# Kernel optimization log

Measured on AMD Instinct MI355X. Metric: run time of the kernel, lower is better.

The kernel has to match this reference:

```python
import jax, jax.numpy as jnp
import numpy as np

D_MODEL = 2048
D_HEAD = 128
N_HEADS = D_MODEL // D_HEAD
SEQ_LENS = (512, 768, 384, 384)  # packed varlen sequences, sum = 2048
L_TOTAL = sum(SEQ_LENS)
EPS = 1e-6


def setup_inputs() -> dict:
    key = jax.random.key(0)
    ks = jax.random.split(key, 8)
    x = jax.random.normal(ks[0], (L_TOTAL, D_MODEL), jnp.float32)
    # Flux-style rope table: pairwise-duplicated cos/sin, pe = concat([cos, sin], -1) -> (L, 2*d_head)
    half = D_HEAD // 2
    pos = np.arange(L_TOTAL, dtype=np.float32)[:, None]
    freqs = 1.0 / (10000.0 ** (np.arange(half, dtype=np.float32) / half))  # (half,)
    ang = pos * freqs[None, :]                      # (L, half)
    cos = np.repeat(np.cos(ang), 2, axis=-1)        # (L, d_head), duplicated per pair
    sin = np.repeat(np.sin(ang), 2, axis=-1)
    pe = jnp.asarray(np.concatenate([cos, sin], axis=-1))  # (L, 2*d_head)
    seq_lens = jnp.asarray(SEQ_LENS, dtype=jnp.int32)
    std = 0.02
    qkv_w = std * jax.random.truncated_normal(ks[1], -2.0, 2.0, (3 * D_MODEL, D_MODEL), jnp.float32)
    qkv_b = jnp.zeros((3 * D_MODEL,), jnp.float32)
    q_scale = jnp.ones((D_HEAD,), jnp.float32)
    k_scale = jnp.ones((D_HEAD,), jnp.float32)
    proj_w = std * jax.random.truncated_normal(ks[2], -2.0, 2.0, (D_MODEL, D_MODEL), jnp.float32)
    proj_b = jnp.zeros((D_MODEL,), jnp.float32)
    return {"x": x, "pe": pe, "seq_lens": seq_lens, "qkv_w": qkv_w, "qkv_b": qkv_b,
            "q_scale": q_scale, "k_scale": k_scale, "proj_w": proj_w, "proj_b": proj_b}


def _rms_norm(t, scale):
    tf = t.astype(jnp.float32)
    rrms = jax.lax.rsqrt(jnp.mean(tf * tf, axis=-1, keepdims=True) + EPS)
    return (tf * rrms * scale).astype(t.dtype)


def _apply_rope(t, pe):
    # t: (L, nh, dh); pe: (L, 2*dh) with pairwise-duplicated cos|sin
    L, nh, dh = t.shape
    c = pe[:, None, 0:dh:2]     # (L, 1, dh/2) per-pair cos
    s = pe[:, None, dh::2]      # (L, 1, dh/2) per-pair sin
    tr = t.reshape(L, nh, dh // 2, 2)
    t1, t2 = tr[..., 0], tr[..., 1]
    out = jnp.stack([t1 * c - t2 * s, t1 * s + t2 * c], axis=-1)
    return out.reshape(L, nh, dh)


def reference(x, pe, seq_lens, qkv_w, qkv_b, q_scale, k_scale, proj_w, proj_b):
    L = x.shape[0]
    qkv = x @ qkv_w.T + qkv_b                      # (L, 3*D)
    q, k, v = jnp.split(qkv, 3, axis=-1)
    q = q.reshape(L, N_HEADS, D_HEAD)
    k = k.reshape(L, N_HEADS, D_HEAD)
    v = v.reshape(L, N_HEADS, D_HEAD)
    q = _rms_norm(q, q_scale)
    k = _rms_norm(k, k_scale)
    q = _apply_rope(q, pe)
    k = _apply_rope(k, pe)
    # block-diagonal (packed varlen) attention
    n = seq_lens.shape[0]
    seg = jnp.repeat(jnp.arange(n, dtype=jnp.int32), seq_lens, total_repeat_length=L)  # (L,)
    mask = seg[:, None] == seg[None, :]            # (L, L) block-diagonal
    scale = 1.0 / jnp.sqrt(jnp.float32(D_HEAD))
    scores = jnp.einsum('lhd,mhd->hlm', q, k) * scale  # (nh, L, L)
    scores = jnp.where(mask[None], scores, jnp.finfo(scores.dtype).min)
    p = jax.nn.softmax(scores, axis=-1)
    out = jnp.einsum('hlm,mhd->lhd', p, v)         # (L, nh, dh)
    out = out.reshape(L, D_MODEL)
    return out @ proj_w.T + proj_b
```

## Files before the change

kernel.cpp:

```cpp
#include <hip/hip_runtime.h>

typedef unsigned short ushort_t;
typedef __attribute__((ext_vector_type(4))) float f4;
typedef __attribute__((ext_vector_type(8))) short s8v;
typedef __attribute__((ext_vector_type(8))) __bf16 bf8v;

#define AS1 __attribute__((address_space(1)))
#define AS3 __attribute__((address_space(3)))

__device__ __forceinline__ void async16(void* lds, const void* g) {
    __builtin_amdgcn_global_load_lds((AS1 const void*)g, (AS3 void*)lds, 16, 0, 0);
}

__device__ __forceinline__ f4 mfma16(s8v a, s8v b, f4 c) {
    return __builtin_amdgcn_mfma_f32_16x16x32_bf16(
        __builtin_bit_cast(bf8v, a), __builtin_bit_cast(bf8v, b), c, 0, 0, 0);
}

__device__ __forceinline__ ushort_t f2bf(float f) {
    unsigned int u = __float_as_uint(f);
    u += 0x7fffu + ((u >> 16) & 1u);
    return (ushort_t)(u >> 16);
}
__device__ __forceinline__ float bf2f(ushort_t u) {
    return __uint_as_float(((unsigned int)u) << 16);
}

#define L_TOT   2048
#define DMODEL  2048
#define DHEAD   128
#define NHEADS  16

__global__ __launch_bounds__(256) void cast_all(const float* __restrict__ x,
                                                const float* __restrict__ w1,
                                                const float* __restrict__ w2,
                                                ushort_t* __restrict__ xo,
                                                ushort_t* __restrict__ w1o,
                                                ushort_t* __restrict__ w2o) {
    int i = blockIdx.x * 256 + threadIdx.x;
    const float* src; ushort_t* dst; int off;
    if (i < 1048576)      { src = x;  dst = xo;  off = 0; }
    else if (i < 4194304) { src = w1; dst = w1o; off = 1048576; }
    else                  { src = w2; dst = w2o; off = 4194304; }
    int j = i - off;
    float4 v = ((const float4*)src)[j];
    ushort4 o;
    o.x = f2bf(v.x); o.y = f2bf(v.y); o.z = f2bf(v.z); o.w = f2bf(v.w);
    ((ushort4*)dst)[j] = o;
}


template <int P>
__device__ __forceinline__ void cluster(f4 (&acc)[8][4], const s8v (&af)[2][2],
                                        const s8v (&bf)[4][2]) {
    __builtin_amdgcn_s_setprio(1);
#pragma unroll
    for (int mm = 0; mm < 2; mm++)
#pragma unroll
        for (int nn = 0; nn < 4; nn++) {
            acc[2 * P + mm][nn] = mfma16(af[mm][0], bf[nn][0], acc[2 * P + mm][nn]);
            acc[2 * P + mm][nn] = mfma16(af[mm][1], bf[nn][1], acc[2 * P + mm][nn]);
        }
    __builtin_amdgcn_s_setprio(0);
}

#define LDF(base, row, oo) (*(const s8v*)&(base)[(row) * 64 + (oo)])

#define STG(dst, gb, Tt, h)                                                              \
    async16(&(dst)[tid * 8 + (2 * (h)) * 4096],                                          \
            (gb) + (size_t)(Tt) * 64 + (size_t)(128 * (h)) * K);                         \
    async16(&(dst)[tid * 8 + (2 * (h) + 1) * 4096],                                      \
            (gb) + (size_t)(Tt) * 64 + (size_t)(128 * (h) + 64) * K);

#define TILE(cur, T)                                                                     \
    {                                                                                    \
        const int Tn1 = ((T) + 1 < NT) ? (T) + 1 : NT - 1;                               \
        const int Tn2 = ((T) + 2 < NT) ? (T) + 2 : NT - 1;                               \
        const ushort_t* fA = stA[cur];                                                   \
        const ushort_t* fB = stB[cur];                                                   \
        s8v bfrag[4][2];                                                                 \
        s8v afrag[2][2];                                                                 \
                                                                  \
        bfrag[0][0] = LDF(fB, brow + 0,  o0); bfrag[0][1] = LDF(fB, brow + 0,  o1);      \
        bfrag[1][0] = LDF(fB, brow + 16, o0); bfrag[1][1] = LDF(fB, brow + 16, o1);      \
        bfrag[2][0] = LDF(fB, brow + 32, o0); bfrag[2][1] = LDF(fB, brow + 32, o1);      \
        bfrag[3][0] = LDF(fB, brow + 48, o0); bfrag[3][1] = LDF(fB, brow + 48, o1);      \
        afrag[0][0] = LDF(fA, arow + 0,  o0); afrag[0][1] = LDF(fA, arow + 0,  o1);      \
        afrag[1][0] = LDF(fA, arow + 16, o0); afrag[1][1] = LDF(fA, arow + 16, o1);      \
        STG(stA[(cur) ^ 1], gA, Tn1, 0)                                                  \
        __builtin_amdgcn_s_barrier();                                                    \
        cluster<0>(acc, afrag, bfrag);                                                   \
        __builtin_amdgcn_s_barrier();                                                    \
                                                                  \
        afrag[0][0] = LDF(fA, arow + 32, o0); afrag[0][1] = LDF(fA, arow + 32, o1);      \
        afrag[1][0] = LDF(fA, arow + 48, o0); afrag[1][1] = LDF(fA, arow + 48, o1);      \
        STG(stA[(cur) ^ 1], gA, Tn1, 1)                                                  \
        __builtin_amdgcn_s_barrier();                                                    \
        cluster<1>(acc, afrag, bfrag);                                                   \
        __builtin_amdgcn_s_barrier();                                                    \
                                                                  \
        afrag[0][0] = LDF(fA, arow + 64, o0); afrag[0][1] = LDF(fA, arow + 64, o1);      \
        afrag[1][0] = LDF(fA, arow + 80, o0); afrag[1][1] = LDF(fA, arow + 80, o1);      \
        STG(stB[cur], gB, Tn2, 0)                                                        \
        __builtin_amdgcn_s_barrier();                                                    \
        cluster<2>(acc, afrag, bfrag);                                                   \
        __builtin_amdgcn_s_barrier();                                                    \
                                                                  \
        afrag[0][0] = LDF(fA, arow + 96,  o0); afrag[0][1] = LDF(fA, arow + 96,  o1);    \
        afrag[1][0] = LDF(fA, arow + 112, o0); afrag[1][1] = LDF(fA, arow + 112, o1);    \
        STG(stB[cur], gB, Tn2, 1)                                                        \
        asm volatile("s_waitcnt vmcnt(4)" ::: "memory");                                 \
        __builtin_amdgcn_sched_barrier(0);                                               \
        __builtin_amdgcn_s_barrier();                                                    \
        cluster<3>(acc, afrag, bfrag);                                                   \
        __builtin_amdgcn_s_barrier();                                                    \
    }

__global__ __launch_bounds__(512, 2) void gemm_qkv256(const ushort_t* __restrict__ A,
                                                      const ushort_t* __restrict__ Bt,
                                                      const float* __restrict__ bias,
                                                      ushort_t* __restrict__ qk_out,
                                                      ushort_t* __restrict__ vt_out,
                                                      int K) {
    __shared__ alignas(16) ushort_t sA[2][16384];
    __shared__ alignas(16) ushort_t sB[2][16384];

    const int tid  = threadIdx.x;
    const int lane = tid & 63;
    const int wave = tid >> 6;
    const int wm = wave >> 2;
    const int wn = wave & 3;
    const int bm = blockIdx.x * 256;
    const int bn = blockIdx.y * 256;
    const bool is_v = blockIdx.y >= 16;
    const int NT = K >> 6;

    const int q15 = lane & 15;
    const int g   = lane >> 4;
    const int l7  = lane & 7;
    const int o0  = ((g    ) ^ l7) * 8;
    const int o1  = ((g + 4) ^ l7) * 8;
    const int arow = wm * 128 + q15;
    const int brow = wn * 64 + q15;

    const int rs  = tid >> 3;
    const int csw = ((tid & 7) ^ (rs & 7)) * 8;
    const ushort_t* Abase = A  + (size_t)(bm + rs) * K + csw;
    const ushort_t* Bbase = Bt + (size_t)(bn + rs) * K + csw;

    ushort_t* stA[2]; ushort_t* stB[2];
    const ushort_t* gA; const ushort_t* gB;
    if (!is_v) { stA[0] = sA[0]; stA[1] = sA[1]; stB[0] = sB[0]; stB[1] = sB[1];
                 gA = Abase; gB = Bbase; }
    else       { stA[0] = sB[0]; stA[1] = sB[1]; stB[0] = sA[0]; stB[1] = sA[1];
                 gA = Bbase; gB = Abase; }

    f4 acc[8][4];
#pragma unroll
    for (int i = 0; i < 8; i++)
#pragma unroll
        for (int j = 0; j < 4; j++) acc[i][j] = (f4){0.f, 0.f, 0.f, 0.f};

    STG(stA[0], gA, 0, 0) STG(stA[0], gA, 0, 1)
    STG(stB[0], gB, 0, 0) STG(stB[0], gB, 0, 1)
    {
        const int T1 = NT > 1 ? 1 : 0;
        STG(stB[1], gB, T1, 0) STG(stB[1], gB, T1, 1)
    }
    asm volatile("s_waitcnt vmcnt(4)" ::: "memory");
    __builtin_amdgcn_sched_barrier(0);
    __builtin_amdgcn_s_barrier();

    for (int T = 0; T < NT; T += 2) {
        TILE(0, T)
        TILE(1, T + 1)
    }

    if (!is_v) {
#pragma unroll
        for (int n = 0; n < 4; n++) {
            int col = bn + wn * 64 + n * 16 + q15;
            float bv = bias[col];
#pragma unroll
            for (int m = 0; m < 8; m++) {
                int r0 = bm + wm * 128 + m * 16 + g * 4;
#pragma unroll
                for (int r = 0; r < 4; r++)
                    qk_out[(size_t)(r0 + r) * 4096 + col] = f2bf(acc[m][n][r] + bv);
            }
        }
    } else {
        const int cb   = (blockIdx.y - 16) * 256 + wm * 128;
        const int tok0 = bm + wn * 64 + q15;
#pragma unroll
        for (int m = 0; m < 8; m++) {
#pragma unroll
            for (int r = 0; r < 4; r++) {
                int c = cb + m * 16 + g * 4 + r;
                float bv = bias[4096 + c];
#pragma unroll
                for (int n = 0; n < 4; n++)
                    vt_out[(size_t)c * L_TOT + tok0 + n * 16] = f2bf(acc[m][n][r] + bv);
            }
        }
    }
}

__global__ __launch_bounds__(256) void gemm_proj(const ushort_t* __restrict__ A,
                                                 const ushort_t* __restrict__ Bt,
                                                 float* __restrict__ Cf,
                                                 int K) {
    __shared__ alignas(16) ushort_t pA[128 * 64];
    __shared__ alignas(16) ushort_t pB[128 * 64];
    const int tid  = threadIdx.x;
    const int lane = tid & 63;
    const int wave = tid >> 6;
    const int wr = (wave >> 1) * 64;
    const int wc = (wave & 1) * 64;
    const int bm = blockIdx.x * 128;
    const int bn = blockIdx.y * 128;

    f4 acc[4][4];
#pragma unroll
    for (int i = 0; i < 4; i++)
#pragma unroll
        for (int j = 0; j < 4; j++) acc[i][j] = (f4){0.f, 0.f, 0.f, 0.f};

    const int rs  = tid >> 3;
    const int csw = ((tid & 7) ^ (rs & 7)) * 8;
    const ushort_t* Abase = A  + (size_t)(bm + rs) * K + csw;
    const ushort_t* Bbase = Bt + (size_t)(bn + rs) * K + csw;
    const int arow = wr + (lane & 15);
    const int brow = wc + (lane & 15);
    const int l7 = lane & 7;
    const int o0 = (((lane >> 4)    ) ^ l7) * 8;
    const int o1 = (((lane >> 4) + 4) ^ l7) * 8;
    const int kbeg = blockIdx.z * (K >> 1);
    const int kend = kbeg + (K >> 1);

    for (int k0 = kbeg; k0 < kend; k0 += 64) {
#pragma unroll
        for (int s = 0; s < 4; s++) {
            async16(&pA[tid * 8 + s * 2048], Abase + k0 + (size_t)(32 * s) * K);
            async16(&pB[tid * 8 + s * 2048], Bbase + k0 + (size_t)(32 * s) * K);
        }
        __syncthreads();

        s8v af[4], bfr[4];
#pragma unroll
        for (int i = 0; i < 4; i++) af[i]  = *(const s8v*)&pA[(arow + i * 16) * 64 + o0];
#pragma unroll
        for (int j = 0; j < 4; j++) bfr[j] = *(const s8v*)&pB[(brow + j * 16) * 64 + o0];
#pragma unroll
        for (int i = 0; i < 4; i++)
#pragma unroll
            for (int j = 0; j < 4; j++) acc[i][j] = mfma16(af[i], bfr[j], acc[i][j]);

#pragma unroll
        for (int i = 0; i < 4; i++) af[i]  = *(const s8v*)&pA[(arow + i * 16) * 64 + o1];
#pragma unroll
        for (int j = 0; j < 4; j++) bfr[j] = *(const s8v*)&pB[(brow + j * 16) * 64 + o1];
#pragma unroll
        for (int i = 0; i < 4; i++)
#pragma unroll
            for (int j = 0; j < 4; j++) acc[i][j] = mfma16(af[i], bfr[j], acc[i][j]);
        __syncthreads();
    }

    const int q = lane & 15;
    const int g = lane >> 4;
    const int crow0 = bm + wr + g * 4;
    const int ccol0 = bn + wc + q;
    float* Cp = Cf + (size_t)blockIdx.z * L_TOT * DMODEL;
#pragma unroll
    for (int j = 0; j < 4; j++) {
        int col = ccol0 + j * 16;
#pragma unroll
        for (int i = 0; i < 4; i++) {
#pragma unroll
            for (int r = 0; r < 4; r++)
                Cp[(size_t)(crow0 + i * 16 + r) * DMODEL + col] = acc[i][j][r];
        }
    }
}

__global__ __launch_bounds__(256) void reduce_bias(const float* __restrict__ part,
                                                   const float* __restrict__ bias,
                                                   float* __restrict__ out) {
    int i = blockIdx.x * 256 + threadIdx.x;
    f4 a = ((const f4*)part)[i];
    f4 b = ((const f4*)(part + (size_t)L_TOT * DMODEL))[i];
    f4 bv = ((const f4*)bias)[i & 511];
    ((f4*)out)[i] = a + b + bv;
}

__global__ __launch_bounds__(256) void norm_rope(const ushort_t* __restrict__ qk,
                                                 const float* __restrict__ pe,
                                                 const float* __restrict__ q_scale,
                                                 const float* __restrict__ k_scale,
                                                 ushort_t* __restrict__ qh,
                                                 ushort_t* __restrict__ kh) {
    int wid  = blockIdx.x * 4 + (threadIdx.x >> 6);
    int lane = threadIdx.x & 63;
    int l = wid >> 4;
    int h = wid & 15;

    const ushort_t* base = qk + (size_t)l * 4096 + h * DHEAD + 2 * lane;
    ushort2 qu = *(const ushort2*)base;
    ushort2 ku = *(const ushort2*)(base + 2048);
    float qvx = bf2f(qu.x), qvy = bf2f(qu.y);
    float kvx = bf2f(ku.x), kvy = bf2f(ku.y);

    float qss = qvx * qvx + qvy * qvy;
    float kss = kvx * kvx + kvy * kvy;
#pragma unroll
    for (int m = 32; m >= 1; m >>= 1) {
        qss += __shfl_xor(qss, m);
        kss += __shfl_xor(kss, m);
    }
    float qr = rsqrtf(qss * (1.0f / DHEAD) + 1e-6f);
    float kr = rsqrtf(kss * (1.0f / DHEAD) + 1e-6f);

    float c = pe[(size_t)l * 256 + 2 * lane];
    float s = pe[(size_t)l * 256 + 128 + 2 * lane];

    float q1 = qvx * qr * q_scale[2 * lane];
    float q2 = qvy * qr * q_scale[2 * lane + 1];
    float k1 = kvx * kr * k_scale[2 * lane];
    float k2 = kvy * kr * k_scale[2 * lane + 1];

    const float sc = 0.08838834764831845f;
    float qo0 = (q1 * c - q2 * s) * sc;
    float qo1 = (q1 * s + q2 * c) * sc;
    float ko0 = k1 * c - k2 * s;
    float ko1 = k1 * s + k2 * c;

    size_t o = ((size_t)h * L_TOT + l) * DHEAD + 2 * lane;
    ushort2 qp, kp;
    qp.x = f2bf(qo0); qp.y = f2bf(qo1);
    kp.x = f2bf(ko0); kp.y = f2bf(ko1);
    *(ushort2*)(qh + o) = qp;
    *(ushort2*)(kh + o) = kp;
}

__global__ __launch_bounds__(256) void attn_kernel(const ushort_t* __restrict__ qh,
                                                   const ushort_t* __restrict__ kh,
                                                   const ushort_t* __restrict__ vt,
                                                   ushort_t* __restrict__ attn_out) {
    __shared__ alignas(16) ushort_t sK[64 * 128];
    __shared__ alignas(16) ushort_t sV[128 * 64];
    __shared__ alignas(16) ushort_t sP[4][16 * 64];

    const int qt = blockIdx.x;
    const int h  = blockIdx.y;
    const int tid = threadIdx.x;
    const int lane = tid & 63;
    const int w = tid >> 6;
    const int qrow0 = qt * 64 + w * 16;

    int q0 = qt * 64;
    int seg_start, seg_end;
    if (q0 < 512)       { seg_start = 0;    seg_end = 512;  }
    else if (q0 < 1280) { seg_start = 512;  seg_end = 1280; }
    else if (q0 < 1664) { seg_start = 1280; seg_end = 1664; }
    else                { seg_start = 1664; seg_end = 2048; }

    const int g = lane >> 4;
    const int q = lane & 15;
    const int qa7 = q & 7;

    const ushort_t* ksrc[4];
    const ushort_t* vsrc[4];
#pragma unroll
    for (int i = 0; i < 4; i++) {
        int p = i * 256 + tid;
        ksrc[i] = kh + ((size_t)h * L_TOT + (p >> 4)) * DHEAD + ((p & 15) ^ ((p >> 4) & 7)) * 8;
        vsrc[i] = vt + ((size_t)h * DHEAD + (p >> 3)) * L_TOT + ((p & 7) ^ ((p >> 3) & 7)) * 8;
    }

    s8v qf[4];
    {
        const ushort_t* qbase = qh + ((size_t)h * L_TOT + qrow0 + q) * DHEAD;
#pragma unroll
        for (int kd = 0; kd < 4; kd++) qf[kd] = *(const s8v*)(qbase + kd * 32 + g * 8);
    }

    f4 o[8];
#pragma unroll
    for (int j = 0; j < 8; j++) o[j] = (f4){0.f, 0.f, 0.f, 0.f};
    float lsum[4] = {0.f, 0.f, 0.f, 0.f};

    for (int kt = seg_start; kt < seg_end; kt += 64) {
#pragma unroll
        for (int i = 0; i < 4; i++) {
            int p = i * 256 + tid;
            async16(&sK[p * 8], ksrc[i] + (size_t)kt * DHEAD);
            async16(&sV[p * 8], vsrc[i] + kt);
        }
        __syncthreads();

        f4 S[4];
#pragma unroll
        for (int tj = 0; tj < 4; tj++) {
            f4 st = (f4){0.f, 0.f, 0.f, 0.f};
#pragma unroll
            for (int kd = 0; kd < 4; kd++) {
                s8v bfrag = *(const s8v*)&sK[(tj * 16 + q) * 128 + (((kd * 4 + g) ^ qa7) * 8)];
                st = mfma16(qf[kd], bfrag, st);
            }
            S[tj] = st;
        }

#pragma unroll
        for (int tj = 0; tj < 4; tj++)
#pragma unroll
            for (int r = 0; r < 4; r++) {
                float p = __expf(S[tj][r]);
                S[tj][r] = p;
                lsum[r] += p;
            }

#pragma unroll
        for (int tj = 0; tj < 4; tj++) {
            int cg = tj * 2 + (q >> 3);
#pragma unroll
            for (int r = 0; r < 4; r++) {
                int prow = g * 4 + r;
                sP[w][prow * 64 + ((cg ^ (prow & 7)) * 8) + qa7] = f2bf(S[tj][r]);
            }
        }
        asm volatile("s_waitcnt lgkmcnt(0)" ::: "memory");

#pragma unroll
        for (int ks = 0; ks < 2; ks++) {
            s8v pf = *(const s8v*)&sP[w][q * 64 + (((ks * 4 + g) ^ qa7) * 8)];
#pragma unroll
            for (int j = 0; j < 8; j++) {
                s8v vf = *(const s8v*)&sV[(j * 16 + q) * 64 + (((ks * 4 + g) ^ qa7) * 8)];
                o[j] = mfma16(pf, vf, o[j]);
            }
        }
        __syncthreads();
    }

#pragma unroll
    for (int r = 0; r < 4; r++) {
        float rs = lsum[r];
        rs += __shfl_xor(rs, 1);
        rs += __shfl_xor(rs, 2);
        rs += __shfl_xor(rs, 4);
        rs += __shfl_xor(rs, 8);
        int row = qrow0 + g * 4 + r;
        float inv = 1.0f / rs;
#pragma unroll
        for (int j = 0; j < 8; j++) {
            attn_out[(size_t)row * DMODEL + h * DHEAD + j * 16 + q] = f2bf(o[j][r] * inv);
        }
    }
}

extern "C" void kernel_launch(void* const* d_in, const int* in_sizes, int n_in,
                              void* d_out, int out_size, void* d_ws, size_t ws_size,
                              hipStream_t stream) {
    const float* x       = (const float*)d_in[0];
    const float* pe      = (const float*)d_in[1];
    const float* qkv_w   = (const float*)d_in[3];
    const float* qkv_b   = (const float*)d_in[4];
    const float* q_scale = (const float*)d_in[5];
    const float* k_scale = (const float*)d_in[6];
    const float* proj_w  = (const float*)d_in[7];
    const float* proj_b  = (const float*)d_in[8];
    float* out = (float*)d_out;

    char* ws = (char*)d_ws;
    const size_t MB = 1024 * 1024;
    ushort_t* x_bf     = (ushort_t*)(ws + 0);
    ushort_t* wqkv_bf  = (ushort_t*)(ws + 8 * MB);
    ushort_t* wproj_bf = (ushort_t*)(ws + 32 * MB);
    ushort_t* qk_bf    = (ushort_t*)(ws + 40 * MB);
    ushort_t* qh       = (ushort_t*)(ws + 57 * MB);
    ushort_t* kh       = (ushort_t*)(ws + 65 * MB);
    ushort_t* vt       = (ushort_t*)(ws + 73 * MB);
    ushort_t* attn_b   = (ushort_t*)(ws + 81 * MB);
    float*    part     = (float*)   (ws + 40 * MB);

    cast_all<<<20480, 256, 0, stream>>>(x, qkv_w, proj_w, x_bf, wqkv_bf, wproj_bf);

    gemm_qkv256<<<dim3(8, 24), 512, 0, stream>>>(x_bf, wqkv_bf, qkv_b, qk_bf, vt, 2048);

    norm_rope<<<8192, 256, 0, stream>>>(qk_bf, pe, q_scale, k_scale, qh, kh);

    attn_kernel<<<dim3(32, 16), 256, 0, stream>>>(qh, kh, vt, attn_b);

    gemm_proj<<<dim3(16, 16, 2), 256, 0, stream>>>(attn_b, wproj_bf, part, 2048);
    reduce_bias<<<4096, 256, 0, stream>>>(part, proj_b, out);
}
```

Measured before the change: 260.9 us.

## Remap block IDs across XCDs, drop split-K in proj GEMM, add LDS waits

Workgroup IDs in the QKV GEMM, proj GEMM and attention kernels are remapped so that consecutive logical tiles land on the same XCD (stride-8 interleave), which should improve L2 reuse of shared A/B panels. The projection GEMM no longer splits K into two partial buffers followed by a reduce kernel. It now runs the full K loop and adds the bias in its epilogue, removing one launch and the fp32 partial round-trip, at the cost of half as many blocks (256). The QKV GEMM tile macro also adds an explicit lgkmcnt(0) wait plus a scheduling barrier after each barrier before the MFMA clusters.

```diff
diff --git a/kernel.cpp b/kernel.cpp
--- a/kernel.cpp
+++ b/kernel.cpp
@@ -72,6 +72,11 @@
     async16(&(dst)[tid * 8 + (2 * (h) + 1) * 4096],                                      \
             (gb) + (size_t)(Tt) * 64 + (size_t)(128 * (h) + 64) * K);
 
+#define OPENB()                                                                          \
+    __builtin_amdgcn_s_barrier();                                                        \
+    asm volatile("s_waitcnt lgkmcnt(0)" ::: "memory");                                   \
+    __builtin_amdgcn_sched_barrier(0);
+
 #define TILE(cur, T)                                                                     \
     {                                                                                    \
         const int Tn1 = ((T) + 1 < NT) ? (T) + 1 : NT - 1;                               \
@@ -88,21 +93,21 @@
         afrag[0][0] = LDF(fA, arow + 0,  o0); afrag[0][1] = LDF(fA, arow + 0,  o1);      \
         afrag[1][0] = LDF(fA, arow + 16, o0); afrag[1][1] = LDF(fA, arow + 16, o1);      \
         STG(stA[(cur) ^ 1], gA, Tn1, 0)                                                  \
-        __builtin_amdgcn_s_barrier();                                                    \
+        OPENB()                                                                          \
         cluster<0>(acc, afrag, bfrag);                                                   \
         __builtin_amdgcn_s_barrier();                                                    \
                                                                   \
         afrag[0][0] = LDF(fA, arow + 32, o0); afrag[0][1] = LDF(fA, arow + 32, o1);      \
         afrag[1][0] = LDF(fA, arow + 48, o0); afrag[1][1] = LDF(fA, arow + 48, o1);      \
         STG(stA[(cur) ^ 1], gA, Tn1, 1)                                                  \
-        __builtin_amdgcn_s_barrier();                                                    \
+        OPENB()                                                                          \
         cluster<1>(acc, afrag, bfrag);                                                   \
         __builtin_amdgcn_s_barrier();                                                    \
                                                                   \
         afrag[0][0] = LDF(fA, arow + 64, o0); afrag[0][1] = LDF(fA, arow + 64, o1);      \
         afrag[1][0] = LDF(fA, arow + 80, o0); afrag[1][1] = LDF(fA, arow + 80, o1);      \
         STG(stB[cur], gB, Tn2, 0)                                                        \
-        __builtin_amdgcn_s_barrier();                                                    \
+        OPENB()                                                                          \
         cluster<2>(acc, afrag, bfrag);                                                   \
         __builtin_amdgcn_s_barrier();                                                    \
                                                                   \
@@ -111,7 +116,7 @@
         STG(stB[cur], gB, Tn2, 1)                                                        \
         asm volatile("s_waitcnt vmcnt(4)" ::: "memory");                                 \
         __builtin_amdgcn_sched_barrier(0);                                               \
-        __builtin_amdgcn_s_barrier();                                                    \
+        OPENB()                                                                          \
         cluster<3>(acc, afrag, bfrag);                                                   \
         __builtin_amdgcn_s_barrier();                                                    \
     }
@@ -130,9 +135,15 @@
     const int wave = tid >> 6;
     const int wm = wave >> 2;
     const int wn = wave & 3;
-    const int bm = blockIdx.x * 256;
-    const int bn = blockIdx.y * 256;
-    const bool is_v = blockIdx.y >= 16;
+
+    const int phys = blockIdx.y * 8 + blockIdx.x;
+    const int lid  = (phys & 7) * 24 + (phys >> 3);
+    const int bxs  = lid & 7;
+    const int bys  = lid >> 3;
+
+    const int bm = bxs * 256;
+    const int bn = bys * 256;
+    const bool is_v = bys >= 16;
     const int NT = K >> 6;
 
     const int q15 = lane & 15;
@@ -190,7 +201,7 @@
             }
         }
     } else {
-        const int cb   = (blockIdx.y - 16) * 256 + wm * 128;
+        const int cb   = (bys - 16) * 256 + wm * 128;
         const int tok0 = bm + wn * 64 + q15;
 #pragma unroll
         for (int m = 0; m < 8; m++) {
@@ -208,7 +219,8 @@
 
 __global__ __launch_bounds__(256) void gemm_proj(const ushort_t* __restrict__ A,
                                                  const ushort_t* __restrict__ Bt,
-                                                 float* __restrict__ Cf,
+                                                 const float* __restrict__ bias,
+                                                 float* __restrict__ out,
                                                  int K) {
     __shared__ alignas(16) ushort_t pA[128 * 64];
     __shared__ alignas(16) ushort_t pB[128 * 64];
@@ -217,8 +229,11 @@
     const int wave = tid >> 6;
     const int wr = (wave >> 1) * 64;
     const int wc = (wave & 1) * 64;
-    const int bm = blockIdx.x * 128;
-    const int bn = blockIdx.y * 128;
+
+    const int phys = blockIdx.y * 16 + blockIdx.x;
+    const int lid  = (phys & 7) * 32 + (phys >> 3);
+    const int bm = (lid & 15) * 128;
+    const int bn = (lid >> 4) * 128;
 
     f4 acc[4][4];
 #pragma unroll
@@ -235,10 +250,8 @@
     const int l7 = lane & 7;
     const int o0 = (((lane >> 4)    ) ^ l7) * 8;
     const int o1 = (((lane >> 4) + 4) ^ l7) * 8;
-    const int kbeg = blockIdx.z * (K >> 1);
-    const int kend = kbeg + (K >> 1);
-
-    for (int k0 = kbeg; k0 < kend; k0 += 64) {
+
+    for (int k0 = 0; k0 < K; k0 += 64) {
 #pragma unroll
         for (int s = 0; s < 4; s++) {
             async16(&pA[tid * 8 + s * 2048], Abase + k0 + (size_t)(32 * s) * K);
@@ -271,27 +284,17 @@
     const int g = lane >> 4;
     const int crow0 = bm + wr + g * 4;
     const int ccol0 = bn + wc + q;
-    float* Cp = Cf + (size_t)blockIdx.z * L_TOT * DMODEL;
 #pragma unroll
     for (int j = 0; j < 4; j++) {
         int col = ccol0 + j * 16;
+        float bv = bias[col];
 #pragma unroll
         for (int i = 0; i < 4; i++) {
 #pragma unroll
             for (int r = 0; r < 4; r++)
-                Cp[(size_t)(crow0 + i * 16 + r) * DMODEL + col] = acc[i][j][r];
-        }
-    }
-}
-
-__global__ __launch_bounds__(256) void reduce_bias(const float* __restrict__ part,
-                                                   const float* __restrict__ bias,
-                                                   float* __restrict__ out) {
-    int i = blockIdx.x * 256 + threadIdx.x;
-    f4 a = ((const f4*)part)[i];
-    f4 b = ((const f4*)(part + (size_t)L_TOT * DMODEL))[i];
-    f4 bv = ((const f4*)bias)[i & 511];
-    ((f4*)out)[i] = a + b + bv;
+                out[(size_t)(crow0 + i * 16 + r) * DMODEL + col] = acc[i][j][r] + bv;
+        }
+    }
 }
 
 __global__ __launch_bounds__(256) void norm_rope(const ushort_t* __restrict__ qk,
@@ -351,8 +354,11 @@
     __shared__ alignas(16) ushort_t sV[128 * 64];
     __shared__ alignas(16) ushort_t sP[4][16 * 64];
 
-    const int qt = blockIdx.x;
-    const int h  = blockIdx.y;
+    const int phys = blockIdx.y * 32 + blockIdx.x;
+    const int lid  = (phys & 7) * 64 + (phys >> 3);
+    const int qt = lid & 31;
+    const int h  = lid >> 5;
+
     const int tid = threadIdx.x;
     const int lane = tid & 63;
     const int w = tid >> 6;
@@ -482,7 +488,6 @@
     ushort_t* kh       = (ushort_t*)(ws + 65 * MB);
     ushort_t* vt       = (ushort_t*)(ws + 73 * MB);
     ushort_t* attn_b   = (ushort_t*)(ws + 81 * MB);
-    float*    part     = (float*)   (ws + 40 * MB);
 
     cast_all<<<20480, 256, 0, stream>>>(x, qkv_w, proj_w, x_bf, wqkv_bf, wproj_bf);
 
@@ -492,6 +497,5 @@
 
     attn_kernel<<<dim3(32, 16), 256, 0, stream>>>(qh, kh, vt, attn_b);
 
-    gemm_proj<<<dim3(16, 16, 2), 256, 0, stream>>>(attn_b, wproj_bf, part, 2048);
-    reduce_bias<<<4096, 256, 0, stream>>>(part, proj_b, out);
-}
+    gemm_proj<<<dim3(16, 16), 256, 0, stream>>>(attn_b, wproj_bf, proj_b, out, 2048);
+}
```

Result: no change. 262.0 us (+0.4%).
